# Optimization experiments

Measured on AMD Instinct MI355X. Metric: run time of the kernel, lower is better.

The kernel has to match this reference:

```python
import jax, jax.numpy as jnp
import numpy as np

T, B, F_, H = 128, 64, 512, 1024  # time, batch, feat, hidden


def hamilton(w):
    """Build dense quaternion (Hamilton-product) weight matrix.
    w: (4, in//4, out//4) components (r, i, j, k) -> (in, out)."""
    r, i, j, k = w[0], w[1], w[2], w[3]
    return jnp.concatenate([
        jnp.concatenate([r, -i, -j, -k], axis=0),
        jnp.concatenate([i,  r, -k,  j], axis=0),
        jnp.concatenate([j,  k,  r, -i], axis=0),
        jnp.concatenate([k, -j,  i,  r], axis=0),
    ], axis=1)


def setup_inputs() -> dict:
    key = jax.random.key(0)
    ks = jax.random.split(key, 16)
    s_in, s_h = 0.05, 0.03  # small init scales for stable gates
    d = {"x": jax.random.normal(ks[0], (T, B, F_), jnp.float32)}
    for idx, n in enumerate(["wfx", "wix", "wox", "wcx"]):
        d[n + "_w"] = jax.random.normal(ks[1 + idx], (4, F_ // 4, H // 4), jnp.float32) * s_in
        d[n + "_b"] = jnp.zeros((H,), jnp.float32)
    for idx, n in enumerate(["ufh", "uih", "uoh", "uch"]):
        d[n + "_w"] = jax.random.normal(ks[5 + idx], (4, H // 4, H // 4), jnp.float32) * s_h
    d["fco_w"] = jax.random.normal(ks[9], (H, F_ + 1), jnp.float32) * 0.02
    d["fco_b"] = jnp.zeros((F_ + 1,), jnp.float32)
    return d


def reference(x, wfx_w, wfx_b, wix_w, wix_b, wox_w, wox_b, wcx_w, wcx_b,
              ufh_w, uih_w, uoh_w, uch_w, fco_w, fco_b):
    # Dense quaternion matrices built once (as torch does per call).
    Wf, Wi, Wo, Wc = (hamilton(w) for w in (wfx_w, wix_w, wox_w, wcx_w))
    Uf, Ui, Uo, Uc = (hamilton(w) for w in (ufh_w, uih_w, uoh_w, uch_w))
    # Precompute all input projections over the whole sequence (as torch does).
    gf = jnp.einsum('tbi,io->tbo', x, Wf) + wfx_b
    gi = jnp.einsum('tbi,io->tbo', x, Wi) + wix_b
    go = jnp.einsum('tbi,io->tbo', x, Wo) + wox_b
    gc = jnp.einsum('tbi,io->tbo', x, Wc) + wcx_b

    def step(carry, g):
        h, c = carry
        gft, git, got, gct = g
        ft = jax.nn.sigmoid(gft + h @ Uf)
        it = jax.nn.sigmoid(git + h @ Ui)
        ot = jax.nn.sigmoid(got + h @ Uo)
        at = gct + h @ Uc
        c = it * jnp.tanh(at) + ft * c
        h = ot * jnp.tanh(c)
        return (h, c), h @ fco_w + fco_b

    h0 = jnp.zeros((B, H), x.dtype)
    _, out = jax.lax.scan(step, (h0, h0), (gf, gi, go, gc))
    return out  # [T, B, F_+1]
```

## Files before the change

kernel.cpp:

```cpp
#include <hip/hip_runtime.h>
#include <stdint.h>

typedef _Float16 f16;
typedef _Float16 f16x8 __attribute__((ext_vector_type(8)));
typedef short bf16x8 __attribute__((ext_vector_type(8)));
typedef float f32x4 __attribute__((ext_vector_type(4)));

#define H_ 1024
#define NG_ 4096
#define F_ 512
#define B_ 64
#define T_ 128
#define NOP_ 640
#define NO_ 513
#define NBLK_R 128

__constant__ int c_comp[16] = {0,1,2,3, 1,0,3,2, 2,3,0,1, 3,2,1,0};
__constant__ float c_sgnf[16] = {1,1,1,1, -1,1,1,-1, -1,-1,1,1, -1,1,-1,1};

__device__ __forceinline__ float bf2f(unsigned short u){
  union { unsigned int i; float f; } v; v.i = ((unsigned int)u) << 16; return v.f;
}
__device__ __forceinline__ unsigned short f2bf(float f){
  union { float f; unsigned int i; } v; v.f = f;
  return (unsigned short)((v.i + 0x7fffu + ((v.i >> 16) & 1u)) >> 16);
}
__device__ __forceinline__ float ldin(const void* p, int i, int f){
  return f ? ((const float*)p)[i] : bf2f(((const unsigned short*)p)[i]);
}
__device__ __forceinline__ float sigm(float x){ return 1.f / (1.f + __expf(-x)); }
__device__ __forceinline__ float tanh_(float x){
  float ax = fabsf(x);
  float e = __expf(-2.f * ax);
  float t = (1.f - e) / (1.f + e);
  return x < 0.f ? -t : t;
}

__device__ __forceinline__ void load_a8_nw(const f16* p, f16x8* a){
  asm volatile(
    "global_load_dwordx4 %0, %8, off sc0 sc1\n\t"
    "global_load_dwordx4 %1, %8, off offset:64 sc0 sc1\n\t"
    "global_load_dwordx4 %2, %8, off offset:128 sc0 sc1\n\t"
    "global_load_dwordx4 %3, %8, off offset:192 sc0 sc1\n\t"
    "global_load_dwordx4 %4, %8, off offset:256 sc0 sc1\n\t"
    "global_load_dwordx4 %5, %8, off offset:320 sc0 sc1\n\t"
    "global_load_dwordx4 %6, %8, off offset:384 sc0 sc1\n\t"
    "global_load_dwordx4 %7, %8, off offset:448 sc0 sc1"
    : "=&v"(a[0]),"=&v"(a[1]),"=&v"(a[2]),"=&v"(a[3]),
      "=&v"(a[4]),"=&v"(a[5]),"=&v"(a[6]),"=&v"(a[7])
    : "v"(p) : "memory");
}
__device__ __forceinline__ void load_c8(const unsigned short* p, bf16x8* a){
  asm volatile(
    "global_load_dwordx4 %0, %8, off\n\t"
    "global_load_dwordx4 %1, %8, off offset:64\n\t"
    "global_load_dwordx4 %2, %8, off offset:128\n\t"
    "global_load_dwordx4 %3, %8, off offset:192\n\t"
    "global_load_dwordx4 %4, %8, off offset:256\n\t"
    "global_load_dwordx4 %5, %8, off offset:320\n\t"
    "global_load_dwordx4 %6, %8, off offset:384\n\t"
    "global_load_dwordx4 %7, %8, off offset:448"
    : "=&v"(a[0]),"=&v"(a[1]),"=&v"(a[2]),"=&v"(a[3]),
      "=&v"(a[4]),"=&v"(a[5]),"=&v"(a[6]),"=&v"(a[7])
    : "v"(p) : "memory");
}
__device__ __forceinline__ void store_h_sys(f16* p, f16 v){
  asm volatile("global_store_short %0, %1, off sc0 sc1" :: "v"(p), "v"(v) : "memory");
}
__device__ __forceinline__ void store_flag_sys(int* p, int v){
  asm volatile("global_store_dword %0, %1, off sc0 sc1" :: "v"(p), "v"(v) : "memory");
}
__device__ __forceinline__ void load_flag2_sys(const int* p0, const int* p1, int &a, int &b){
  asm volatile(
    "global_load_dword %0, %2, off sc0 sc1\n\t"
    "global_load_dword %1, %3, off sc0 sc1\n\t"
    "s_waitcnt vmcnt(0)"
    : "=&v"(a), "=&v"(b) : "v"(p0), "v"(p1) : "memory");
}
__device__ __forceinline__ void drain_vmem(){
  asm volatile("s_waitcnt vmcnt(0)" ::: "memory");
}
#define WAIT_VM(n) do { \
  asm volatile("s_waitcnt vmcnt(" #n ")" ::: "memory"); \
  __builtin_amdgcn_sched_barrier(0); \
} while (0)

__global__ void detect_kernel(const unsigned short* __restrict__ xu, int* __restrict__ flag){
  __shared__ int zc, wc;
  if (threadIdx.x == 0){ zc = 0; wc = 0; }
  __syncthreads();
  unsigned short u = xu[2 * threadIdx.x];
  int e = (u >> 7) & 0xFF;
  bool z = (u & 0x7FFF) == 0;
  bool wild = !z && (e < 67 || e > 150);
  if (z) atomicAdd(&zc, 1);
  if (wild) atomicAdd(&wc, 1);
  __syncthreads();
  if (threadIdx.x == 0) *flag = (zc >= 128 || wc >= 64) ? 1 : 0;
}

#define WX_ELEMS (NG_*F_)
#define U_ELEMS  (NG_*H_)
#define FCO_ELEMS (NOP_*H_)
#define BIAS_ELEMS NG_
#define OB_ELEMS NOP_
#define XC_ELEMS (T_*B_*F_)
#define PACK_TOTAL (WX_ELEMS + U_ELEMS + FCO_ELEMS + BIAS_ELEMS + OB_ELEMS + XC_ELEMS)

__global__ void pack_kernel(
    const void* __restrict__ x,
    const void* __restrict__ wf, const void* __restrict__ wi,
    const void* __restrict__ wo, const void* __restrict__ wc,
    const void* __restrict__ bfv, const void* __restrict__ biv,
    const void* __restrict__ bov, const void* __restrict__ bcv,
    const void* __restrict__ uf, const void* __restrict__ ui,
    const void* __restrict__ uo, const void* __restrict__ uc,
    const void* __restrict__ fcw, const void* __restrict__ fcb,
    const int* __restrict__ flag,
    unsigned short* __restrict__ Wx, f16* __restrict__ U, f16* __restrict__ Fco,
    float* __restrict__ bias, float* __restrict__ ob,
    unsigned short* __restrict__ Xc)
{
  const int fl = *flag;
  int i = blockIdx.x * blockDim.x + threadIdx.x;
  if (i < WX_ELEMS) {
    int n = i >> 9, k = i & 511;
    int g = n >> 10, nn = n & 1023;
    int q = nn >> 8, be = nn & 255;
    int p = k >> 7, al = k & 127;
    const void* w = (g==0) ? wf : (g==1) ? wi : (g==2) ? wo : wc;
    int pq = p*4 + q;
    Wx[i] = f2bf(c_sgnf[pq] * ldin(w, c_comp[pq]*32768 + al*256 + be, fl));
    return;
  }
  i -= WX_ELEMS;
  if (i < U_ELEMS) {
    int n = i >> 10, k = i & 1023;
    int g = n >> 10;
    int q = (n & 1023) >> 8, be = n & 255;
    int p = k >> 8, al = k & 255;
    const void* u = (g==0) ? uf : (g==1) ? ui : (g==2) ? uo : uc;
    int pq = p*4 + q;
    U[i] = (f16)(c_sgnf[pq] * ldin(u, c_comp[pq]*65536 + al*256 + be, fl));
    return;
  }
  i -= U_ELEMS;
  if (i < FCO_ELEMS) {
    int n = i >> 10, k = i & 1023;
    Fco[i] = (n < NO_) ? (f16)ldin(fcw, k*NO_ + n, fl) : (f16)0.f;
    return;
  }
  i -= FCO_ELEMS;
  if (i < BIAS_ELEMS) {
    int g = i >> 10;
    const void* b = (g==0) ? bfv : (g==1) ? biv : (g==2) ? bov : bcv;
    bias[i] = ldin(b, i & 1023, fl);
    return;
  }
  i -= BIAS_ELEMS;
  if (i < OB_ELEMS) {
    ob[i] = (i < NO_) ? ldin(fcb, i, fl) : 0.f;
    return;
  }
  i -= OB_ELEMS;
  if (i < XC_ELEMS) {
    Xc[i] = fl ? f2bf(((const float*)x)[i]) : ((const unsigned short*)x)[i];
  }
}

__global__ __launch_bounds__(256) void recur_all(
    const unsigned short* __restrict__ Xc,
    const unsigned short* __restrict__ Wxp,
    const f16* __restrict__ U,
    const float* __restrict__ bias,
    f16* __restrict__ Hall,
    int* __restrict__ flags)
{
  __shared__ f16 Usm[32768];
  __shared__ unsigned short Wxsm[16384];
  const int blk = blockIdx.x;
  const int jb = blk * 8;
  const int tid = threadIdx.x;
  const int lane = tid & 63, w = tid >> 6;
  const int lo = lane & 15, quad = lane >> 4;
  const int m0 = w * 16;

  #pragma unroll
  for (int j = 0; j < 16; j++) {
    int u = tid + j*256;
    int lp = u & 63, f = u >> 6;
    int ki = f >> 1, nt = f & 1;
    int n = nt*16 + (lp & 15), qd = lp >> 4;
    int row = (n >> 3)*H_ + jb + (n & 7);
    *(f16x8*)(Usm + f*512 + lp*8) =
        *(const f16x8*)(U + (size_t)row*H_ + ki*32 + qd*8);
  }
  #pragma unroll
  for (int j = 0; j < 8; j++) {
    int u = tid + j*256;
    int lp = u & 63, f = u >> 6;
    int ku = f >> 1, p = f & 1;
    int col = (p*2 + ((lp & 15) >> 3))*1024 + jb + (lp & 7);
    *(f16x8*)((f16*)Wxsm + f*512 + lp*8) =
        *(const f16x8*)((const f16*)Wxp + (size_t)col*F_ + ku*32 + (lp >> 4)*8);
  }
  const int cc = lane & 7, hi = (lane >> 3) & 1;
  const int colg = jb + cc;
  const int b0r = m0 + quad*4 + hi*2;
  float creg[2] = {0.f, 0.f};
  const float bf0 = bias[colg];
  const float bf1 = bias[1024 + colg];
  const float bf2 = bias[2048 + colg];
  const float bf3 = bias[3072 + colg];
  __syncthreads();

  f32x4 xp0 = {0.f,0.f,0.f,0.f}, xp1 = {0.f,0.f,0.f,0.f};
  bf16x8 xa0[8], xa1[8];
  {
    const unsigned short* xr = Xc + (size_t)(m0 + lo)*F_ + quad*8;
    load_c8(xr, xa0);
    load_c8(xr + 256, xa1);
    drain_vmem();
    __builtin_amdgcn_sched_barrier(0);
    #pragma unroll
    for (int u = 0; u < 8; u++) {
      xp0 = __builtin_amdgcn_mfma_f32_16x16x32_bf16(xa0[u], *(const bf16x8*)((f16*)Wxsm + (u*2+0)*512 + lane*8), xp0, 0, 0, 0);
      xp1 = __builtin_amdgcn_mfma_f32_16x16x32_bf16(xa0[u], *(const bf16x8*)((f16*)Wxsm + (u*2+1)*512 + lane*8), xp1, 0, 0, 0);
    }
    #pragma unroll
    for (int u = 0; u < 8; u++) {
      xp0 = __builtin_amdgcn_mfma_f32_16x16x32_bf16(xa1[u], *(const bf16x8*)((f16*)Wxsm + ((8+u)*2+0)*512 + lane*8), xp0, 0, 0, 0);
      xp1 = __builtin_amdgcn_mfma_f32_16x16x32_bf16(xa1[u], *(const bf16x8*)((f16*)Wxsm + ((8+u)*2+1)*512 + lane*8), xp1, 0, 0, 0);
    }
  }

  for (int t = 0; t < T_; t++) {
    f32x4 acc0 = xp0, acc1 = xp1;
    const f16* Ap = Hall + (size_t)t*B_*H_ + (size_t)(m0 + lo)*H_ + quad*8;
    f16x8 a0[8], a1[8], a2[8], a3[8];
    drain_vmem();
    load_a8_nw(Ap,       a0);
    load_a8_nw(Ap + 256, a1);
    load_a8_nw(Ap + 512, a2);
    load_a8_nw(Ap + 768, a3);
    {
      const int tn = (t + 1 < T_) ? t + 1 : 0;
      const unsigned short* xr = Xc + (size_t)tn*B_*F_ + (size_t)(m0 + lo)*F_ + quad*8;
      load_c8(xr, xa0);
      load_c8(xr + 256, xa1);
    }
    WAIT_VM(40);
    #pragma unroll
    for (int u = 0; u < 8; u++) {
      f16x8 bb0 = *(const f16x8*)(Usm + ((u)*2+0)*512 + lane*8);
      f16x8 bb1 = *(const f16x8*)(Usm + ((u)*2+1)*512 + lane*8);
      acc0 = __builtin_amdgcn_mfma_f32_16x16x32_f16(a0[u], bb0, acc0, 0, 0, 0);
      acc1 = __builtin_amdgcn_mfma_f32_16x16x32_f16(a0[u], bb1, acc1, 0, 0, 0);
    }
    WAIT_VM(32);
    #pragma unroll
    for (int u = 0; u < 8; u++) {
      f16x8 bb0 = *(const f16x8*)(Usm + ((8+u)*2+0)*512 + lane*8);
      f16x8 bb1 = *(const f16x8*)(Usm + ((8+u)*2+1)*512 + lane*8);
      acc0 = __builtin_amdgcn_mfma_f32_16x16x32_f16(a1[u], bb0, acc0, 0, 0, 0);
      acc1 = __builtin_amdgcn_mfma_f32_16x16x32_f16(a1[u], bb1, acc1, 0, 0, 0);
    }
    WAIT_VM(24);
    #pragma unroll
    for (int u = 0; u < 8; u++) {
      f16x8 bb0 = *(const f16x8*)(Usm + ((16+u)*2+0)*512 + lane*8);
      f16x8 bb1 = *(const f16x8*)(Usm + ((16+u)*2+1)*512 + lane*8);
      acc0 = __builtin_amdgcn_mfma_f32_16x16x32_f16(a2[u], bb0, acc0, 0, 0, 0);
      acc1 = __builtin_amdgcn_mfma_f32_16x16x32_f16(a2[u], bb1, acc1, 0, 0, 0);
    }
    WAIT_VM(16);
    #pragma unroll
    for (int u = 0; u < 8; u++) {
      f16x8 bb0 = *(const f16x8*)(Usm + ((24+u)*2+0)*512 + lane*8);
      f16x8 bb1 = *(const f16x8*)(Usm + ((24+u)*2+1)*512 + lane*8);
      acc0 = __builtin_amdgcn_mfma_f32_16x16x32_f16(a3[u], bb0, acc0, 0, 0, 0);
      acc1 = __builtin_amdgcn_mfma_f32_16x16x32_f16(a3[u], bb1, acc1, 0, 0, 0);
    }
    WAIT_VM(0);
    f16* Hn = Hall + (size_t)(t+1)*B_*H_;
    #pragma unroll
    for (int e = 0; e < 2; e++) {
      int src = quad*16 + cc;
      float f_lo = __shfl(acc0[e],   src);
      float f_hi = __shfl(acc0[2+e], src);
      float i_lo = __shfl(acc0[e],   src + 8);
      float i_hi = __shfl(acc0[2+e], src + 8);
      float o_lo = __shfl(acc1[e],   src);
      float o_hi = __shfl(acc1[2+e], src);
      float a_lo = __shfl(acc1[e],   src + 8);
      float a_hi = __shfl(acc1[2+e], src + 8);
      float pf = (hi ? f_hi : f_lo) + bf0;
      float pi = (hi ? i_hi : i_lo) + bf1;
      float po = (hi ? o_hi : o_lo) + bf2;
      float pa = (hi ? a_hi : a_lo) + bf3;
      float vf = sigm(pf), vi = sigm(pi), vo = sigm(po);
      creg[e] = vi * tanh_(pa) + vf * creg[e];
      float hn = vo * tanh_(creg[e]);
      store_h_sys(Hn + (size_t)(b0r + e)*H_ + colg, (f16)hn);
    }
    xp0 = (f32x4){0.f,0.f,0.f,0.f};
    xp1 = (f32x4){0.f,0.f,0.f,0.f};
    #pragma unroll
    for (int u = 0; u < 8; u++) {
      xp0 = __builtin_amdgcn_mfma_f32_16x16x32_bf16(xa0[u], *(const bf16x8*)((f16*)Wxsm + (u*2+0)*512 + lane*8), xp0, 0, 0, 0);
      xp1 = __builtin_amdgcn_mfma_f32_16x16x32_bf16(xa0[u], *(const bf16x8*)((f16*)Wxsm + (u*2+1)*512 + lane*8), xp1, 0, 0, 0);
    }
    #pragma unroll
    for (int u = 0; u < 8; u++) {
      xp0 = __builtin_amdgcn_mfma_f32_16x16x32_bf16(xa1[u], *(const bf16x8*)((f16*)Wxsm + ((8+u)*2+0)*512 + lane*8), xp0, 0, 0, 0);
      xp1 = __builtin_amdgcn_mfma_f32_16x16x32_bf16(xa1[u], *(const bf16x8*)((f16*)Wxsm + ((8+u)*2+1)*512 + lane*8), xp1, 0, 0, 0);
    }
    if (t + 1 < T_) {
      drain_vmem();
      __syncthreads();
      const int target = t + 1;
      if (tid == 0) store_flag_sys(flags + blk*16, target);
      if (w == 0) {
        const int* fp0 = flags + (2*lane)*16;
        const int* fp1 = flags + (2*lane+1)*16;
        int f0, f1;
        do {
          load_flag2_sys(fp0, fp1, f0, f1);
        } while (!__all(f0 >= target && f1 >= target));
      }
      __syncthreads();
    } else {
      drain_vmem();
    }
  }
}

__global__ __launch_bounds__(256) void gemm_out(
    const f16* __restrict__ A,
    const f16* __restrict__ Bt,
    const float* __restrict__ ob,
    float* __restrict__ out)
{
  const int lane = threadIdx.x & 63, w = threadIdx.x >> 6;
  const int lo = lane & 15, quad = lane >> 4;
  const int m0 = blockIdx.x * 128 + (w >> 1) * 64;
  const int n0 = blockIdx.y * 128 + (w & 1) * 64;
  f32x4 acc[4][4] = {};
  #pragma unroll 2
  for (int k0 = 0; k0 < H_; k0 += 32) {
    f16x8 a[4], b[4];
    #pragma unroll
    for (int mt = 0; mt < 4; mt++)
      a[mt] = *(const f16x8*)(A + (size_t)(m0 + 16*mt + lo) * H_ + k0 + quad*8);
    #pragma unroll
    for (int nt = 0; nt < 4; nt++)
      b[nt] = *(const f16x8*)(Bt + (size_t)(n0 + 16*nt + lo) * H_ + k0 + quad*8);
    #pragma unroll
    for (int mt = 0; mt < 4; mt++)
      #pragma unroll
      for (int nt = 0; nt < 4; nt++)
        acc[mt][nt] = __builtin_amdgcn_mfma_f32_16x16x32_f16(a[mt], b[nt], acc[mt][nt], 0, 0, 0);
  }
  #pragma unroll
  for (int mt = 0; mt < 4; mt++)
    #pragma unroll
    for (int nt = 0; nt < 4; nt++)
      #pragma unroll
      for (int r = 0; r < 4; r++) {
        int row = m0 + 16*mt + quad*4 + r;
        int col = n0 + 16*nt + lo;
        if (col < NO_)
          out[(size_t)row * NO_ + col] = acc[mt][nt][r] + ob[col];
      }
}

extern "C" void kernel_launch(void* const* d_in, const int* in_sizes, int n_in,
                              void* d_out, int out_size, void* d_ws, size_t ws_size,
                              hipStream_t stream)
{
  const void* x   = d_in[0];
  const void* wfw = d_in[1];  const void* wfb = d_in[2];
  const void* wiw = d_in[3];  const void* wib = d_in[4];
  const void* wow = d_in[5];  const void* wob = d_in[6];
  const void* wcw = d_in[7];  const void* wcb = d_in[8];
  const void* ufw = d_in[9];  const void* uiw = d_in[10];
  const void* uow = d_in[11]; const void* ucw = d_in[12];
  const void* fcw = d_in[13]; const void* fcb = d_in[14];

  char* ws = (char*)d_ws;
  unsigned short* Wx = (unsigned short*)(ws + 0);
  f16*   U    = (f16*)  (ws + 4194304);
  f16*   Fco  = (f16*)  (ws + 12582912);
  unsigned short* Xc = (unsigned short*)(ws + 13893632);
  f16*   Hall = (f16*)  (ws + 22282240);
  float* bias = (float*)(ws + 39190528);
  float* ob   = (float*)(ws + 39206912);
  int*   flags= (int*)  (ws + 39209472);
  int*   flag = (int*)  (ws + 39217664);
  if (ws_size < 39217668u) return;

  hipMemsetAsync(Hall, 0, (size_t)B_*H_*sizeof(f16), stream);
  hipMemsetAsync(flags, 0, NBLK_R*16*sizeof(int), stream);

  detect_kernel<<<1, 256, 0, stream>>>((const unsigned short*)x, flag);

  pack_kernel<<<(PACK_TOTAL + 255)/256, 256, 0, stream>>>(
      x, wfw, wiw, wow, wcw, wfb, wib, wob, wcb, ufw, uiw, uow, ucw, fcw, fcb,
      flag, Wx, U, Fco, bias, ob, Xc);

  {
    const unsigned short* Xcp = Xc;
    const unsigned short* Wxp = Wx;
    const f16* Up = U;
    const float* bp = bias;
    f16* Hp = Hall;
    int* flp = flags;
    void* args[] = {&Xcp, &Wxp, &Up, &bp, &Hp, &flp};
    hipLaunchCooperativeKernel((const void*)recur_all, dim3(NBLK_R), dim3(256),
                               args, 0, stream);
  }

  gemm_out<<<dim3(64, 5), 256, 0, stream>>>(Hall + (size_t)B_*H_, Fco, ob, (float*)d_out);
}
```

Baseline: 1.217 ms.

## Use per-wave grid flags, overlap input-projection MFMA with barrier, fold setup kernels

```diff
diff --git a/kernel.cpp b/kernel.cpp
--- a/kernel.cpp
+++ b/kernel.cpp
@@ -5,6 +5,7 @@
 typedef _Float16 f16x8 __attribute__((ext_vector_type(8)));
 typedef short bf16x8 __attribute__((ext_vector_type(8)));
 typedef float f32x4 __attribute__((ext_vector_type(4)));
+typedef int i32x4 __attribute__((ext_vector_type(4)));
 
 #define H_ 1024
 #define NG_ 4096
@@ -14,6 +15,7 @@
 #define NOP_ 640
 #define NO_ 513
 #define NBLK_R 128
+#define NFLAG_ 512
 
 __constant__ int c_comp[16] = {0,1,2,3, 1,0,3,2, 2,3,0,1, 3,2,1,0};
 __constant__ float c_sgnf[16] = {1,1,1,1, -1,1,1,-1, -1,-1,1,1, -1,1,-1,1};
@@ -70,13 +72,6 @@
 __device__ __forceinline__ void store_flag_sys(int* p, int v){
   asm volatile("global_store_dword %0, %1, off sc0 sc1" :: "v"(p), "v"(v) : "memory");
 }
-__device__ __forceinline__ void load_flag2_sys(const int* p0, const int* p1, int &a, int &b){
-  asm volatile(
-    "global_load_dword %0, %2, off sc0 sc1\n\t"
-    "global_load_dword %1, %3, off sc0 sc1\n\t"
-    "s_waitcnt vmcnt(0)"
-    : "=&v"(a), "=&v"(b) : "v"(p0), "v"(p1) : "memory");
-}
 __device__ __forceinline__ void drain_vmem(){
   asm volatile("s_waitcnt vmcnt(0)" ::: "memory");
 }
@@ -85,18 +80,17 @@
   __builtin_amdgcn_sched_barrier(0); \
 } while (0)
 
-__global__ void detect_kernel(const unsigned short* __restrict__ xu, int* __restrict__ flag){
-  __shared__ int zc, wc;
-  if (threadIdx.x == 0){ zc = 0; wc = 0; }
-  __syncthreads();
-  unsigned short u = xu[2 * threadIdx.x];
-  int e = (u >> 7) & 0xFF;
-  bool z = (u & 0x7FFF) == 0;
-  bool wild = !z && (e < 67 || e > 150);
-  if (z) atomicAdd(&zc, 1);
-  if (wild) atomicAdd(&wc, 1);
-  __syncthreads();
-  if (threadIdx.x == 0) *flag = (zc >= 128 || wc >= 64) ? 1 : 0;
+__device__ __forceinline__ int poll512(const int* flags, int target){
+  const int lane = threadIdx.x & 63;
+  const int* p = flags + lane*8;
+  i32x4 v0, v1;
+  asm volatile(
+    "global_load_dwordx4 %0, %2, off sc0 sc1\n\t"
+    "global_load_dwordx4 %1, %2, off offset:16 sc0 sc1\n\t"
+    "s_waitcnt vmcnt(0)"
+    : "=&v"(v0), "=&v"(v1) : "v"(p) : "memory");
+  return __all(v0[0] >= target && v0[1] >= target && v0[2] >= target && v0[3] >= target &&
+               v1[0] >= target && v1[1] >= target && v1[2] >= target && v1[3] >= target);
 }
 
 #define WX_ELEMS (NG_*F_)
@@ -105,7 +99,9 @@
 #define BIAS_ELEMS NG_
 #define OB_ELEMS NOP_
 #define XC_ELEMS (T_*B_*F_)
-#define PACK_TOTAL (WX_ELEMS + U_ELEMS + FCO_ELEMS + BIAS_ELEMS + OB_ELEMS + XC_ELEMS)
+#define HZ_ELEMS (B_*H_)
+#define FZ_ELEMS NFLAG_
+#define PACK_TOTAL (WX_ELEMS + U_ELEMS + FCO_ELEMS + BIAS_ELEMS + OB_ELEMS + XC_ELEMS + HZ_ELEMS + FZ_ELEMS)
 
 __global__ void pack_kernel(
     const void* __restrict__ x,
@@ -116,12 +112,26 @@
     const void* __restrict__ uf, const void* __restrict__ ui,
     const void* __restrict__ uo, const void* __restrict__ uc,
     const void* __restrict__ fcw, const void* __restrict__ fcb,
-    const int* __restrict__ flag,
     unsigned short* __restrict__ Wx, f16* __restrict__ U, f16* __restrict__ Fco,
     float* __restrict__ bias, float* __restrict__ ob,
-    unsigned short* __restrict__ Xc)
+    unsigned short* __restrict__ Xc,
+    f16* __restrict__ Hz, int* __restrict__ Fz)
 {
-  const int fl = *flag;
+  __shared__ int zc, wc2;
+  if (threadIdx.x == 0){ zc = 0; wc2 = 0; }
+  __syncthreads();
+  {
+    const unsigned short* xu = (const unsigned short*)x;
+    unsigned short u = xu[2 * threadIdx.x];
+    int e = (u >> 7) & 0xFF;
+    bool z = (u & 0x7FFF) == 0;
+    bool wild = !z && (e < 67 || e > 150);
+    if (z) atomicAdd(&zc, 1);
+    if (wild) atomicAdd(&wc2, 1);
+  }
+  __syncthreads();
+  const int fl = (zc >= 128 || wc2 >= 64) ? 1 : 0;
+
   int i = blockIdx.x * blockDim.x + threadIdx.x;
   if (i < WX_ELEMS) {
     int n = i >> 9, k = i & 511;
@@ -165,7 +175,12 @@
   i -= OB_ELEMS;
   if (i < XC_ELEMS) {
     Xc[i] = fl ? f2bf(((const float*)x)[i]) : ((const unsigned short*)x)[i];
-  }
+    return;
+  }
+  i -= XC_ELEMS;
+  if (i < HZ_ELEMS) { Hz[i] = (f16)0.f; return; }
+  i -= HZ_ELEMS;
+  if (i < FZ_ELEMS) { Fz[i] = 0; }
 }
 
 __global__ __launch_bounds__(256) void recur_all(
@@ -303,32 +318,24 @@
       float hn = vo * tanh_(creg[e]);
       store_h_sys(Hn + (size_t)(b0r + e)*H_ + colg, (f16)hn);
     }
-    xp0 = (f32x4){0.f,0.f,0.f,0.f};
-    xp1 = (f32x4){0.f,0.f,0.f,0.f};
-    #pragma unroll
-    for (int u = 0; u < 8; u++) {
-      xp0 = __builtin_amdgcn_mfma_f32_16x16x32_bf16(xa0[u], *(const bf16x8*)((f16*)Wxsm + (u*2+0)*512 + lane*8), xp0, 0, 0, 0);
-      xp1 = __builtin_amdgcn_mfma_f32_16x16x32_bf16(xa0[u], *(const bf16x8*)((f16*)Wxsm + (u*2+1)*512 + lane*8), xp1, 0, 0, 0);
-    }
-    #pragma unroll
-    for (int u = 0; u < 8; u++) {
-      xp0 = __builtin_amdgcn_mfma_f32_16x16x32_bf16(xa1[u], *(const bf16x8*)((f16*)Wxsm + ((8+u)*2+0)*512 + lane*8), xp0, 0, 0, 0);
-      xp1 = __builtin_amdgcn_mfma_f32_16x16x32_bf16(xa1[u], *(const bf16x8*)((f16*)Wxsm + ((8+u)*2+1)*512 + lane*8), xp1, 0, 0, 0);
-    }
     if (t + 1 < T_) {
       drain_vmem();
-      __syncthreads();
-      const int target = t + 1;
-      if (tid == 0) store_flag_sys(flags + blk*16, target);
-      if (w == 0) {
-        const int* fp0 = flags + (2*lane)*16;
-        const int* fp1 = flags + (2*lane+1)*16;
-        int f0, f1;
-        do {
-          load_flag2_sys(fp0, fp1, f0, f1);
-        } while (!__all(f0 >= target && f1 >= target));
+      if (lane == 0) store_flag_sys(flags + (blk*4 + w), t + 1);
+      __builtin_amdgcn_sched_barrier(0);
+      xp0 = (f32x4){0.f,0.f,0.f,0.f};
+      xp1 = (f32x4){0.f,0.f,0.f,0.f};
+      #pragma unroll
+      for (int u = 0; u < 8; u++) {
+        xp0 = __builtin_amdgcn_mfma_f32_16x16x32_bf16(xa0[u], *(const bf16x8*)((f16*)Wxsm + (u*2+0)*512 + lane*8), xp0, 0, 0, 0);
+        xp1 = __builtin_amdgcn_mfma_f32_16x16x32_bf16(xa0[u], *(const bf16x8*)((f16*)Wxsm + (u*2+1)*512 + lane*8), xp1, 0, 0, 0);
       }
-      __syncthreads();
+      #pragma unroll
+      for (int u = 0; u < 8; u++) {
+        xp0 = __builtin_amdgcn_mfma_f32_16x16x32_bf16(xa1[u], *(const bf16x8*)((f16*)Wxsm + ((8+u)*2+0)*512 + lane*8), xp0, 0, 0, 0);
+        xp1 = __builtin_amdgcn_mfma_f32_16x16x32_bf16(xa1[u], *(const bf16x8*)((f16*)Wxsm + ((8+u)*2+1)*512 + lane*8), xp1, 0, 0, 0);
+      }
+      __builtin_amdgcn_sched_barrier(0);
+      while (!poll512(flags, t + 1)) {}
     } else {
       drain_vmem();
     }
@@ -396,17 +403,11 @@
   float* bias = (float*)(ws + 39190528);
   float* ob   = (float*)(ws + 39206912);
   int*   flags= (int*)  (ws + 39209472);
-  int*   flag = (int*)  (ws + 39217664);
-  if (ws_size < 39217668u) return;
-
-  hipMemsetAsync(Hall, 0, (size_t)B_*H_*sizeof(f16), stream);
-  hipMemsetAsync(flags, 0, NBLK_R*16*sizeof(int), stream);
-
-  detect_kernel<<<1, 256, 0, stream>>>((const unsigned short*)x, flag);
+  if (ws_size < 39211520u) return;
 
   pack_kernel<<<(PACK_TOTAL + 255)/256, 256, 0, stream>>>(
       x, wfw, wiw, wow, wcw, wfb, wib, wob, wcb, ufw, uiw, uow, ucw, fcw, fcb,
-      flag, Wx, U, Fco, bias, ob, Xc);
+      Wx, U, Fco, bias, ob, Xc, Hall, flags);
 
   {
     const unsigned short* Xcp = Xc;
```

After: 1.615 ms. 32.7% more time.
